# Kernel tuning notes

Hardware: AMD Instinct MI355X
Metric: run time of the kernel (lower is better)

The kernel has to match this reference:

```python
import jax, jax.numpy as jnp
import numpy as np

PC_RANGE = [-51.2, -51.2, -5.0, 51.2, 51.2, 3.0]
VOXEL = [0.1, 0.1, 0.2]
OSF = 8
NUM_PRIOR = 100
C = 256
BN_EPS = 1e-5
LN_EPS = 1e-5


def _conv(x, w, pad):
    # x: [B,C,H,W], w: [O,I,kh,kw]
    return jax.lax.conv_general_dilated(
        x, w, window_strides=(1, 1), padding=[(pad, pad), (pad, pad)],
        dimension_numbers=('NCHW', 'OIHW', 'NCHW'))


def _bn(x, g, b, m, v):
    scale = (g / jnp.sqrt(v + BN_EPS))[None, :, None, None]
    return (x - m[None, :, None, None]) * scale + b[None, :, None, None]


def setup_inputs() -> dict:
    key = jax.random.key(0)
    ks = jax.random.split(key, 24)
    s3 = 1.0 / np.sqrt(C * 9)
    s1 = 1.0 / np.sqrt(C)
    inp = {
        'bev_feat': jax.random.normal(ks[0], (4, C, 128, 128), jnp.float32),
        'template_anchor': jax.random.normal(ks[1], (4, 900, 11), jnp.float32),
        # shared_conv: 3x3 conv (no bias) + BN(eval) + ReLU
        'shared_w': jax.random.normal(ks[2], (C, C, 3, 3), jnp.float32) * s3,
        'bn1_g': jax.random.normal(ks[3], (C,), jnp.float32) * 0.1 + 1.0,
        'bn1_b': jax.random.normal(ks[4], (C,), jnp.float32) * 0.1,
        'bn1_m': jax.random.normal(ks[5], (C,), jnp.float32) * 0.1,
        'bn1_v': jax.random.uniform(ks[6], (C,), jnp.float32) + 0.5,
        # objectness: 3x3 conv (no bias) + BN + ReLU + 1x1 conv (bias=-2)
        'obj_w1': jax.random.normal(ks[7], (C, C, 3, 3), jnp.float32) * s3,
        'bn2_g': jax.random.normal(ks[8], (C,), jnp.float32) * 0.1 + 1.0,
        'bn2_b': jax.random.normal(ks[9], (C,), jnp.float32) * 0.1,
        'bn2_m': jax.random.normal(ks[10], (C,), jnp.float32) * 0.1,
        'bn2_v': jax.random.uniform(ks[11], (C,), jnp.float32) + 0.5,
        'obj_w2': jax.random.normal(ks[12], (1, C, 1, 1), jnp.float32) * s1,
        'obj_b2': jnp.full((1,), -2.0, jnp.float32),
        # feat_proj: Linear + LN + ReLU + Linear
        'fp_w1': jax.random.normal(ks[13], (C, C), jnp.float32) * s1,
        'fp_b1': jax.random.normal(ks[14], (C,), jnp.float32) * 0.01,
        'ln_g': jnp.ones((C,), jnp.float32),
        'ln_b': jnp.zeros((C,), jnp.float32),
        'fp_w2': jax.random.normal(ks[15], (C, C), jnp.float32) * s1,
        'fp_b2': jax.random.normal(ks[16], (C,), jnp.float32) * 0.01,
        # geometry heads (1x1 convs, bias init 0)
        'z_w': jax.random.normal(ks[17], (1, C, 1, 1), jnp.float32) * s1,
        'z_b': jnp.zeros((1,), jnp.float32),
        'dim_w': jax.random.normal(ks[18], (3, C, 1, 1), jnp.float32) * s1,
        'dim_b': jnp.zeros((3,), jnp.float32),
        'yaw_w': jax.random.normal(ks[19], (2, C, 1, 1), jnp.float32) * s1,
        'yaw_b': jnp.zeros((2,), jnp.float32),
        'vel_w': jax.random.normal(ks[20], (2, C, 1, 1), jnp.float32) * s1,
        'vel_b': jnp.zeros((2,), jnp.float32),
    }
    return inp


def _forward(bev_feat, template_anchor, shared_w, bn1_g, bn1_b, bn1_m, bn1_v,
             obj_w1, bn2_g, bn2_b, bn2_m, bn2_v, obj_w2, obj_b2,
             fp_w1, fp_b1, ln_g, ln_b, fp_w2, fp_b2,
             z_w, z_b, dim_w, dim_b, yaw_w, yaw_b, vel_w, vel_b):
    B, Cc, H, W = bev_feat.shape
    # shared_conv
    feat = jax.nn.relu(_bn(_conv(bev_feat, shared_w, 1), bn1_g, bn1_b, bn1_m, bn1_v))
    # objectness heatmap
    h = jax.nn.relu(_bn(_conv(feat, obj_w1, 1), bn2_g, bn2_b, bn2_m, bn2_v))
    heatmap = jax.nn.sigmoid(_conv(h, obj_w2, 0) + obj_b2[None, :, None, None])
    score = heatmap.reshape(B, H * W)
    K = min(NUM_PRIOR, H * W, template_anchor.shape[1])
    topk_score, topk_inds = jax.lax.top_k(score, K)  # [B,K]
    ys = topk_inds // W
    xs = topk_inds % W
    # gather BEV features at topk locations: [B,K,C]
    feat_flat = feat.reshape(B, Cc, H * W).transpose(0, 2, 1)
    gathered = jnp.take_along_axis(feat_flat, topk_inds[:, :, None], axis=1)
    # feat_proj: Linear + LN + ReLU + Linear
    x = gathered @ fp_w1.T + fp_b1
    mu = jnp.mean(x, axis=-1, keepdims=True)
    var = jnp.mean((x - mu) ** 2, axis=-1, keepdims=True)
    x = (x - mu) / jnp.sqrt(var + LN_EPS) * ln_g + ln_b
    x = jax.nn.relu(x)
    prior_feature = x @ fp_w2.T + fp_b2
    prior_feature = prior_feature * (1.0 + topk_score[:, :, None])
    # geometry heads (1x1 convs == linear on gathered features)
    z_pred = gathered @ z_w[:, :, 0, 0].T + z_b      # [B,K,1]
    dim_pred = gathered @ dim_w[:, :, 0, 0].T + dim_b  # [B,K,3]
    yaw_pred = gathered @ yaw_w[:, :, 0, 0].T + yaw_b  # [B,K,2]
    vel_pred = gathered @ vel_w[:, :, 0, 0].T + vel_b  # [B,K,2]
    # anchor update
    pa = template_anchor[:, :K, :]
    x_metric = (xs.astype(pa.dtype) + 0.5) * (VOXEL[0] * OSF) + PC_RANGE[0]
    y_metric = (ys.astype(pa.dtype) + 0.5) * (VOXEL[1] * OSF) + PC_RANGE[1]
    z_new = pa[..., 2] + 0.5 * z_pred[..., 0]
    dims_new = pa[..., 3:6] + 0.2 * jnp.clip(dim_pred, -1.0, 1.0)
    yaw = jnp.tanh(yaw_pred)
    nrm = jnp.maximum(jnp.sqrt(jnp.sum(yaw * yaw, axis=-1, keepdims=True)), 1e-6)
    yaw_new = 0.7 * pa[..., 6:8] + 0.3 * (yaw / nrm)
    vel_new = pa[..., 8:10] + 0.2 * jnp.clip(vel_pred, -2.0, 2.0)
    prior_anchor = jnp.concatenate([
        x_metric[..., None], y_metric[..., None], z_new[..., None],
        dims_new, yaw_new, vel_new, pa[..., 10:]], axis=-1)
    return prior_feature, prior_anchor, topk_score


def reference(bev_feat, template_anchor, shared_w, bn1_g, bn1_b, bn1_m, bn1_v,
              obj_w1, bn2_g, bn2_b, bn2_m, bn2_v, obj_w2, obj_b2,
              fp_w1, fp_b1, ln_g, ln_b, fp_w2, fp_b2,
              z_w, z_b, dim_w, dim_b, yaw_w, yaw_b, vel_w, vel_b):
    return _forward(bev_feat, template_anchor, shared_w, bn1_g, bn1_b, bn1_m, bn1_v,
                    obj_w1, bn2_g, bn2_b, bn2_m, bn2_v, obj_w2, obj_b2,
                    fp_w1, fp_b1, ln_g, ln_b, fp_w2, fp_b2,
                    z_w, z_b, dim_w, dim_b, yaw_w, yaw_b, vel_w, vel_b)
```

## Files before the change

### kernel.cpp

```cpp
#include <hip/hip_runtime.h>
#include <math.h>


typedef __attribute__((ext_vector_type(8))) short bf16x8;
typedef __attribute__((ext_vector_type(4))) float f32x4;

#define HW 16384
#define WPITCH 130
#define CCAP 192
#define PSTR 28
#define WSO_XN    0ULL
#define WSO_FEATB 34078720ULL
#define WSO_WP1   68157440ULL
#define WSO_WP2   69337088ULL
#define WSO_BNP   70516736ULL
#define WSO_LOG   70521856ULL
#define WSO_CAND  70784000ULL
#define WSO_CNT   70787072ULL
#define WSO_EXL   70787136ULL
#define WSO_TIDX  70790208ULL
#define WSO_TLOG  70791808ULL
#define WSO_W1N   70793408ULL
#define WSO_W2N   73152704ULL
#define WSO_A1P   WSO_XN
#define WSO_ACC2  28311552ULL

__device__ __forceinline__ float bf2f(short s) {
  return __uint_as_float(((unsigned)(unsigned short)s) << 16);
}
__device__ __forceinline__ short f2bf(float f) {
  unsigned u = __float_as_uint(f);
  u += 0x7fffu + ((u >> 16) & 1u);
  return (short)(u >> 16);
}
__device__ __forceinline__ void gll16(const void* g, void* l) {
  __builtin_amdgcn_global_load_lds(
      (const __attribute__((address_space(1))) void*)g,
      (__attribute__((address_space(3))) void*)l, 16, 0, 0);
}

__global__ void wprep2(const float* __restrict__ s1, const float* __restrict__ s2,
                       short* __restrict__ wp1, short* __restrict__ wp2,
                       float* __restrict__ wn1, float* __restrict__ wn2) {
  int bx = blockIdx.x;
  const float* src;
  short* wp;
  float* wn;
  if (bx >= 2304) {
    src = s2; wp = wp2; wn = wn2; bx -= 2304;
  } else {
    src = s1; wp = wp1; wn = wn1;
  }
  int i = bx * 256 + threadIdx.x;
  float v = src[i];
  int k = i % 9;
  int r = i / 9;
  int ci = r & 255;
  int co = r >> 8;
  wp[(k * 256 + co) * 256 + ci] = f2bf(v);
  wn[(ci * 9 + k) * 256 + co] = v;
}

__global__ void smallprep(const float* g1, const float* b1, const float* m1,
                          const float* v1, const float* g2, const float* b2,
                          const float* m2, const float* v2, const float* w2,
                          const float* ob2, float* __restrict__ bnp,
                          short* __restrict__ xn, short* __restrict__ featb,
                          float* __restrict__ logits) {
  const int blk = blockIdx.x, t = threadIdx.x;
  if (blk < 1024) {
    int i = blk * 256 + t;
    int c = i & 255;
    int r = i >> 8;
    int nh = r >> 1;
    int side = r & 1;
    size_t off = ((size_t)nh * WPITCH + (side ? 129 : 0)) * 256 + c;
    xn[off] = 0;
    featb[off] = 0;
  } else if (blk < 1280) {
    logits[(blk - 1024) * 256 + t] = ob2[0];
  } else {
    float s1 = g1[t] / sqrtf(v1[t] + 1e-5f);
    bnp[t] = s1;
    bnp[256 + t] = b1[t] - m1[t] * s1;
    float s2 = g2[t] / sqrtf(v2[t] + 1e-5f);
    bnp[512 + t] = s2;
    bnp[768 + t] = b2[t] - m2[t] * s2;
    bnp[1024 + t] = w2[t];
  }
}

__global__ __launch_bounds__(256) void nchw2nhwc(const float* __restrict__ in,
                                                 short* __restrict__ out) {
  __shared__ short tl[64 * 66];
  int n = blockIdx.z, c0 = blockIdx.y * 64, s0 = blockIdx.x * 64;
  int sl = threadIdx.x & 63, cl = threadIdx.x >> 6;
  for (int p = 0; p < 16; ++p) {
    int c = cl + p * 4;
    tl[c * 66 + sl] = f2bf(in[(((size_t)(n * 256 + c0 + c)) << 14) + s0 + sl]);
  }
  __syncthreads();
  int co = threadIdx.x & 63, so = threadIdx.x >> 6;
  for (int p = 0; p < 16; ++p) {
    int S = s0 + so + p * 4;
    int h = S >> 7, w = S & 127;
    out[(((size_t)(n * 128 + h)) * WPITCH + w + 1) * 256 + c0 + co] =
        tl[co * 66 + (so + p * 4)];
  }
}

template <int OUT_LOGITS>
__global__ __launch_bounds__(256) void conv3x3(const short* __restrict__ inp,
                                               const short* __restrict__ wp,
                                               const float* __restrict__ scale,
                                               const float* __restrict__ shift,
                                               const float* __restrict__ w2f,
                                               short* __restrict__ outb,
                                               float* __restrict__ logits) {
  __shared__ short a_sm[132 * 32];
  __shared__ short b_sm[3][128 * 32];
  const int t = threadIdx.x;
  const int wv = t >> 6, lane = t & 63;
  const int l15 = lane & 15, quad = lane >> 4;
  const int tile = blockIdx.x;
  const int img = tile >> 7;
  const int h = tile & 127;
  const int nblk = blockIdx.y;
  const int m0 = (wv & 1) << 6;
  const int n0 = (wv >> 1) << 6;

  f32x4 acc[4][4];
#pragma unroll
  for (int i = 0; i < 4; ++i)
#pragma unroll
    for (int j = 0; j < 4; ++j) {
      acc[i][j][0] = 0.f; acc[i][j][1] = 0.f;
      acc[i][j][2] = 0.f; acc[i][j][3] = 0.f;
    }

  for (int dhi = 0; dhi < 3; ++dhi) {
    const int hy = h + dhi - 1;
    if (hy < 0 || hy > 127) continue;
    const size_t arow = ((size_t)(img * 128 + hy)) * WPITCH;
    const short* wbase = wp + ((size_t)(dhi * 3 * 256 + nblk * 128)) * 256;

    for (int c0 = 0; c0 < 256; c0 += 32) {
      __syncthreads();
#pragma unroll
      for (int j = 0; j < 2; ++j) {
        const int seg = (j << 6) + (t >> 2);
        const int cc = t & 3;
        gll16(inp + (arow + seg) * 256 + c0 + cc * 8,
              a_sm + ((size_t)((j << 8) + t)) * 8);
      }
      if (t < 32) {
        const int r = t >> 4, dw = t & 15;
        const int* gsrc = (const int*)(inp + (arow + 128 + r) * 256 + c0) + dw;
        ((int*)a_sm)[(128 + r) * 16 + dw] = *gsrc;
      }
#pragma unroll
      for (int dwi = 0; dwi < 3; ++dwi) {
        const short* wtap = wbase + (size_t)dwi * 65536;
#pragma unroll
        for (int j = 0; j < 2; ++j) {
          const int nrow = (j << 6) + (t >> 2);
          const int cc = t & 3;
          gll16(wtap + (size_t)nrow * 256 + c0 + cc * 8,
                b_sm[dwi] + ((size_t)((j << 8) + t)) * 8);
        }
      }
      __syncthreads();

#pragma unroll
      for (int dwi = 0; dwi < 3; ++dwi) {
        bf16x8 af[4], bfr[4];
#pragma unroll
        for (int i = 0; i < 4; ++i)
          af[i] = *(const bf16x8*)(a_sm + (dwi + m0 + i * 16 + l15) * 32 + quad * 8);
#pragma unroll
        for (int i = 0; i < 4; ++i)
          bfr[i] = *(const bf16x8*)(b_sm[dwi] + (n0 + i * 16 + l15) * 32 + quad * 8);
#pragma unroll
        for (int i = 0; i < 4; ++i)
#pragma unroll
          for (int j = 0; j < 4; ++j)
            acc[i][j] = __builtin_amdgcn_mfma_f32_16x16x32_bf16(af[i], bfr[j],
                                                                acc[i][j], 0, 0, 0);
      }
    }
  }

  float sc[4], sh[4], wf[4];
#pragma unroll
  for (int j = 0; j < 4; ++j) {
    const int co = nblk * 128 + n0 + j * 16 + l15;
    sc[j] = scale[co];
    sh[j] = shift[co];
    if (OUT_LOGITS) wf[j] = w2f[co];
  }
  if (OUT_LOGITS) {
    float* lrow = logits + ((size_t)img << 14) + (h << 7);
#pragma unroll
    for (int i = 0; i < 4; ++i) {
#pragma unroll
      for (int r = 0; r < 4; ++r) {
        float part = 0.f;
#pragma unroll
        for (int j = 0; j < 4; ++j) {
          float v = fmaxf(acc[i][j][r] * sc[j] + sh[j], 0.f);
          part += v * wf[j];
        }
        part += __shfl_xor(part, 1);
        part += __shfl_xor(part, 2);
        part += __shfl_xor(part, 4);
        part += __shfl_xor(part, 8);
        if (l15 == 0)
          atomicAdd(&lrow[m0 + i * 16 + quad * 4 + r], part);
      }
    }
  } else {
    const size_t obase = ((size_t)(img * 128 + h)) * WPITCH + 1;
#pragma unroll
    for (int i = 0; i < 4; ++i) {
#pragma unroll
      for (int j = 0; j < 4; ++j) {
        const int co = nblk * 128 + n0 + j * 16 + l15;
#pragma unroll
        for (int r = 0; r < 4; ++r) {
          const int m = m0 + i * 16 + quad * 4 + r;
          float v = fmaxf(acc[i][j][r] * sc[j] + sh[j], 0.f);
          outb[(obase + m) * 256 + co] = f2bf(v);
        }
      }
    }
  }
}

__global__ __launch_bounds__(1024) void topk_radix(const float* __restrict__ logits,
                                                   int* __restrict__ cand,
                                                   int* __restrict__ cnt_out) {
  __shared__ int hist[2048];
  __shared__ int wsum[16];
  __shared__ unsigned sel_bin;
  __shared__ int sel_above;
  __shared__ int cntr;
  const int b = blockIdx.x, t = threadIdx.x;
  const int lane = t & 63, wid = t >> 6;
  const float* L = logits + (size_t)b * HW;
  const int base = t * 16;
  unsigned kv[16];
#pragma unroll
  for (int i = 0; i < 4; ++i) {
    float4 v = *(const float4*)(L + base + i * 4);
    float f4[4] = {v.x, v.y, v.z, v.w};
#pragma unroll
    for (int j = 0; j < 4; ++j) {
      unsigned u = __float_as_uint(f4[j]);
      kv[i * 4 + j] = u ^ (((unsigned)((int)u >> 31)) | 0x80000000u);
    }
  }
  unsigned prefix = 0, pmask = 0;
  int need = 128;
  const int shifts[3] = {21, 10, 0};
  const int nbs[3] = {2048, 2048, 1024};

  for (int lev = 0; lev < 3; ++lev) {
    const int shift = shifts[lev];
    const int nb = nbs[lev];
    hist[t] = 0;
    hist[t + 1024] = 0;
    __syncthreads();
#pragma unroll
    for (int i = 0; i < 16; ++i)
      if ((kv[i] & pmask) == prefix)
        atomicAdd(&hist[(kv[i] >> shift) & (nb - 1)], 1);
    __syncthreads();
    const int cs = nb >> 10;
    const int bin_hi = nb - 1 - t * cs;
    const int c_hi = hist[bin_hi];
    const int c_lo = (cs == 2) ? hist[bin_hi - 1] : 0;
    const int s = c_hi + c_lo;
    int inc = s;
    for (int off = 1; off < 64; off <<= 1) {
      int nbr = __shfl_up(inc, off);
      if (lane >= off) inc += nbr;
    }
    if (lane == 63) wsum[wid] = inc;
    __syncthreads();
    if (wid == 0) {
      int wv = (lane < 16) ? wsum[lane] : 0;
      for (int off = 1; off < 16; off <<= 1) {
        int nbr = __shfl_up(wv, off);
        if (lane >= off) wv += nbr;
      }
      if (lane < 16) wsum[lane] = wv;
    }
    __syncthreads();
    const int excl = inc - s + (wid ? wsum[wid - 1] : 0);
    if (excl < need && need <= excl + s) {
      if (need <= excl + c_hi) {
        sel_bin = (unsigned)bin_hi;
        sel_above = excl;
      } else {
        sel_bin = (unsigned)(bin_hi - 1);
        sel_above = excl + c_hi;
      }
    }
    __syncthreads();
    prefix |= sel_bin << shift;
    pmask |= ((unsigned)(nb - 1)) << shift;
    need -= sel_above;
    __syncthreads();
  }
  if (t == 0) cntr = 0;
  __syncthreads();
#pragma unroll
  for (int i = 0; i < 16; ++i) {
    if (kv[i] >= prefix) {
      int p = atomicAdd(&cntr, 1);
      if (p < CCAP) cand[b * CCAP + p] = base + i;
    }
  }
  __syncthreads();
  if (t == 0) cnt_out[b] = (cntr < CCAP) ? cntr : CCAP;
}

__global__ __launch_bounds__(256) void rescore_a(const float* __restrict__ bev,
                                                 const float* __restrict__ w1n,
                                                 const int* __restrict__ cand,
                                                 const int* __restrict__ cnt,
                                                 float* __restrict__ a1part) {
  const int bx = blockIdx.x, b = blockIdx.y, z = blockIdx.z;
  const int t = threadIdx.x;
  const int n = cnt[b];
  const int c0 = bx * 4;
  if (c0 >= n) return;
  const int nc = (n - c0 < 4) ? (n - c0) : 4;
  const int ci0 = z << 6;
  __shared__ float patch[4 * 64 * PSTR];

  {
    const int TE = nc * 1600;
    int sg[4];
#pragma unroll
    for (int g = 0; g < 4; ++g) {
      int cc = c0 + g;
      sg[g] = cand[b * CCAP + ((cc < n) ? cc : (n - 1))];
    }
#pragma unroll
    for (int k = 0; k < 25; ++k) {
      int e = t + (k << 8);
      if (e < TE) {
        int g = (e >= 3200) ? ((e >= 4800) ? 3 : 2) : ((e >= 1600) ? 1 : 0);
        int rem = e - g * 1600;
        int ci = rem / 25;
        int rj = rem - ci * 25;
        int r = rj / 5;
        int j = rj - r * 5;
        int s = sg[g];
        int hy = (s >> 7) - 2 + r, wx = (s & 127) - 2 + j;
        float v = 0.f;
        if (hy >= 0 && hy < 128 && wx >= 0 && wx < 128)
          v = bev[(((size_t)(b * 256 + ci0 + ci)) << 14) + (hy << 7) + wx];
        patch[(g * 64 + ci) * PSTR + rj] = v;
      } else {
        int g2 = (e >= 3200) ? ((e >= 4800) ? 3 : 2) : 1;
        int rem = e - g2 * 1600;
        int ci = rem / 25;
        int rj = rem - ci * 25;
        patch[(g2 * 64 + ci) * PSTR + rj] = 0.f;
      }
    }
  }
  __syncthreads();

  const int co = t;
  float a[4][9];
#pragma unroll
  for (int g = 0; g < 4; ++g)
#pragma unroll
    for (int p = 0; p < 9; ++p) a[g][p] = 0.f;

  for (int ci = 0; ci < 64; ++ci) {
    const float* wr = w1n + (size_t)(ci0 + ci) * 2304 + co;
    float w9[9];
#pragma unroll
    for (int k = 0; k < 9; ++k) w9[k] = wr[k * 256];
#pragma unroll
    for (int g = 0; g < 4; ++g) {
      const float4* pr = (const float4*)(patch + (g * 64 + ci) * PSTR);
      float xp[28];
#pragma unroll
      for (int q = 0; q < 7; ++q) {
        float4 v = pr[q];
        xp[q * 4 + 0] = v.x; xp[q * 4 + 1] = v.y;
        xp[q * 4 + 2] = v.z; xp[q * 4 + 3] = v.w;
      }
#pragma unroll
      for (int py = 0; py < 3; ++py)
#pragma unroll
        for (int px = 0; px < 3; ++px)
#pragma unroll
          for (int ky = 0; ky < 3; ++ky)
#pragma unroll
            for (int kx = 0; kx < 3; ++kx)
              a[g][py * 3 + px] += w9[ky * 3 + kx] * xp[(py + ky) * 5 + px + kx];
    }
  }

#pragma unroll
  for (int g = 0; g < 4; ++g) {
    if (g < nc) {
      float* dst =
          a1part + ((((size_t)(b * CCAP + c0 + g) * 4 + z) * 9) << 8) + co;
#pragma unroll
      for (int p = 0; p < 9; ++p) dst[p << 8] = a[g][p];
    }
  }
}

__global__ __launch_bounds__(256) void rescore_b(const float* __restrict__ a1part,
                                                 const float* __restrict__ w2n,
                                                 const float* __restrict__ bnp,
                                                 const int* __restrict__ cnt,
                                                 float* __restrict__ acc2) {
  const int bx = blockIdx.x, b = blockIdx.y, z = blockIdx.z;
  const int t = threadIdx.x;
  const int n = cnt[b];
  const int cbase = bx * 8;
  if (cbase >= n) return;
  const int zb = z << 6;
  __shared__ float f9[8 * 64 * 12];

  const int cf = t & 63;
  const int pg = t >> 6;
  const int cfg = zb + cf;
  const float sc1 = bnp[cfg], sh1 = bnp[256 + cfg];
#pragma unroll
  for (int g = 0; g < 8; ++g) {
    const int c = cbase + g;
    if (c < n) {
      const float* src =
          a1part + ((((size_t)(b * CCAP + c)) * 36) << 8) + cfg;
      for (int p = pg; p < 9; p += 4) {
        float v = src[(size_t)(0 * 9 + p) << 8] + src[(size_t)(1 * 9 + p) << 8] +
                  src[(size_t)(2 * 9 + p) << 8] + src[(size_t)(3 * 9 + p) << 8];
        f9[(g * 64 + cf) * 12 + p] = fmaxf(v * sc1 + sh1, 0.f);
      }
    } else {
      for (int p = pg; p < 9; p += 4) f9[(g * 64 + cf) * 12 + p] = 0.f;
    }
  }
  __syncthreads();

  float acc[8];
#pragma unroll
  for (int g = 0; g < 8; ++g) acc[g] = 0.f;
  for (int ci = 0; ci < 64; ++ci) {
    const float* wr = w2n + (size_t)(zb + ci) * 2304 + t;
    float w9[9];
#pragma unroll
    for (int k = 0; k < 9; ++k) w9[k] = wr[k * 256];
#pragma unroll
    for (int g = 0; g < 8; ++g) {
      const float4* fp = (const float4*)(f9 + (g * 64 + ci) * 12);
      float4 f0 = fp[0], f1 = fp[1], f2 = fp[2];
      acc[g] += w9[0] * f0.x;
      acc[g] += w9[1] * f0.y;
      acc[g] += w9[2] * f0.z;
      acc[g] += w9[3] * f0.w;
      acc[g] += w9[4] * f1.x;
      acc[g] += w9[5] * f1.y;
      acc[g] += w9[6] * f1.z;
      acc[g] += w9[7] * f1.w;
      acc[g] += w9[8] * f2.x;
    }
  }
#pragma unroll
  for (int g = 0; g < 8; ++g) {
    const int c = cbase + g;
    if (c < n)
      acc2[((((size_t)(b * CCAP + c)) * 4 + z) << 8) + t] = acc[g];
  }
}

__global__ __launch_bounds__(256) void rescore_c(const float* __restrict__ acc2,
                                                 const float* __restrict__ bnp,
                                                 const float* __restrict__ b2,
                                                 const int* __restrict__ cnt,
                                                 float* __restrict__ exlog) {
  const int bx = blockIdx.x, b = blockIdx.y, t = threadIdx.x;
  const int lane = t & 63, wid = t >> 6;
  const int n = cnt[b];
  const int c = bx * 4 + wid;
  if (c >= n) return;
  const float* src = acc2 + (((size_t)(b * CCAP + c)) << 10);
  float p = 0.f;
#pragma unroll
  for (int j = 0; j < 4; ++j) {
    const int co = lane + j * 64;
    float v = ((src[co] + src[256 + co]) + src[512 + co]) + src[768 + co];
    p += fmaxf(v * bnp[512 + co] + bnp[768 + co], 0.f) * bnp[1024 + co];
  }
  for (int off = 32; off; off >>= 1) p += __shfl_xor(p, off);
  if (lane == 0) exlog[b * CCAP + c] = p + b2[0];
}

__global__ __launch_bounds__(CCAP) void final_topk(const float* __restrict__ exlog,
                                                   const int* __restrict__ cand,
                                                   const int* __restrict__ cnt,
                                                   int* __restrict__ tidx,
                                                   float* __restrict__ tlog) {
  const int b = blockIdx.x, t = threadIdx.x;
  __shared__ float v[CCAP];
  __shared__ int si[CCAP];
  const int n = cnt[b];
  float mv = (t < n) ? exlog[b * CCAP + t] : -3.0e38f;
  int s = (t < n) ? cand[b * CCAP + t] : 0x7FFFFFFF;
  v[t] = mv;
  si[t] = s;
  __syncthreads();
  int rank = 0;
  for (int j = 0; j < CCAP; ++j) {
    float vj = v[j];
    int sj = si[j];
    if (vj > mv || (vj == mv && sj < s)) ++rank;
  }
  if (t < n && rank < 100) {
    tidx[b * 100 + rank] = s;
    tlog[b * 100 + rank] = mv;
  }
}

__global__ __launch_bounds__(256) void head_kern(
    const short* __restrict__ featb, const int* __restrict__ tidx,
    const float* __restrict__ tlog, const float* __restrict__ tmpl,
    const float* __restrict__ w1, const float* __restrict__ b1,
    const float* __restrict__ lng, const float* __restrict__ lnb,
    const float* __restrict__ w2, const float* __restrict__ b2,
    const float* __restrict__ zw, const float* __restrict__ zb,
    const float* __restrict__ dmw, const float* __restrict__ dmb,
    const float* __restrict__ yw, const float* __restrict__ yb,
    const float* __restrict__ vw, const float* __restrict__ vb,
    float* __restrict__ out) {
  const int blk = blockIdx.x;
  const int b = blk / 100, q = blk % 100;
  const int t = threadIdx.x;
  const int lane = t & 63, wid = t >> 6;
  __shared__ float g[256];
  __shared__ float sx[256];
  __shared__ float red[4];
  __shared__ float heads[8];

  const int s = tidx[b * 100 + q];
  const float score = 1.f / (1.f + expf(-tlog[b * 100 + q]));
  const int ys = s >> 7, xs = s & 127;

  g[t] = bf2f(featb[(((size_t)(b * 128 + ys)) * WPITCH + xs + 1) * 256 + t]);
  __syncthreads();

  float x = b1[t];
  {
    const float* wr = w1 + (size_t)t * 256;
    for (int i = 0; i < 256; i += 4) {
      float4 wv = *(const float4*)(wr + i);
      x += g[i] * wv.x + g[i + 1] * wv.y + g[i + 2] * wv.z + g[i + 3] * wv.w;
    }
  }
  float sum = x;
  for (int off = 32; off; off >>= 1) sum += __shfl_xor(sum, off);
  if (lane == 0) red[wid] = sum;
  __syncthreads();
  float mu = (red[0] + red[1] + red[2] + red[3]) * (1.f / 256.f);
  __syncthreads();
  float d = x - mu;
  float q2 = d * d;
  for (int off = 32; off; off >>= 1) q2 += __shfl_xor(q2, off);
  if (lane == 0) red[wid] = q2;
  __syncthreads();
  float var = (red[0] + red[1] + red[2] + red[3]) * (1.f / 256.f);
  float xn = d * (1.f / sqrtf(var + 1e-5f)) * lng[t] + lnb[t];
  xn = fmaxf(xn, 0.f);
  sx[t] = xn;
  __syncthreads();
  float pf = b2[t];
  {
    const float* wr = w2 + (size_t)t * 256;
    for (int i = 0; i < 256; i += 4) {
      float4 wv = *(const float4*)(wr + i);
      pf += sx[i] * wv.x + sx[i + 1] * wv.y + sx[i + 2] * wv.z + sx[i + 3] * wv.w;
    }
  }
  pf *= (1.f + score);
  out[(size_t)(b * 100 + q) * 256 + t] = pf;

  const int k = t >> 5, l = t & 31;
  const float* hw;
  float hb;
  if (k == 0)      { hw = zw;                 hb = zb[0]; }
  else if (k < 4)  { hw = dmw + (k - 1) * 256; hb = dmb[k - 1]; }
  else if (k < 6)  { hw = yw + (k - 4) * 256;  hb = yb[k - 4]; }
  else             { hw = vw + (k - 6) * 256;  hb = vb[k - 6]; }
  float hp = 0.f;
#pragma unroll
  for (int r = 0; r < 8; ++r) {
    int i = l + r * 32;
    hp += g[i] * hw[i];
  }
  for (int off = 16; off; off >>= 1) hp += __shfl_xor(hp, off);
  if (l == 0) heads[k] = hp + hb;
  __syncthreads();

  if (t == 0) {
    const float* pa = tmpl + ((size_t)b * 900 + q) * 11;
    float p[11];
#pragma unroll
    for (int i = 0; i < 11; ++i) p[i] = pa[i];
    float a[11];
    a[0] = ((float)xs + 0.5f) * 0.8f - 51.2f;
    a[1] = ((float)ys + 0.5f) * 0.8f - 51.2f;
    a[2] = p[2] + 0.5f * heads[0];
#pragma unroll
    for (int i = 0; i < 3; ++i)
      a[3 + i] = p[3 + i] + 0.2f * fminf(fmaxf(heads[1 + i], -1.f), 1.f);
    float t0 = tanhf(heads[4]), t1 = tanhf(heads[5]);
    float nrm = fmaxf(sqrtf(t0 * t0 + t1 * t1), 1e-6f);
    a[6] = 0.7f * p[6] + 0.3f * t0 / nrm;
    a[7] = 0.7f * p[7] + 0.3f * t1 / nrm;
    a[8] = p[8] + 0.2f * fminf(fmaxf(heads[6], -2.f), 2.f);
    a[9] = p[9] + 0.2f * fminf(fmaxf(heads[7], -2.f), 2.f);
    a[10] = p[10];
    float* oa = out + 102400 + (size_t)(b * 100 + q) * 11;
#pragma unroll
    for (int i = 0; i < 11; ++i) oa[i] = a[i];
    out[106800 + b * 100 + q] = score;
  }
}

extern "C" void kernel_launch(void* const* d_in, const int* in_sizes, int n_in,
                              void* d_out, int out_size, void* d_ws, size_t ws_size,
                              hipStream_t stream) {
  (void)in_sizes; (void)n_in; (void)out_size; (void)ws_size;
  char* ws = (char*)d_ws;
  short* xn     = (short*)(ws + WSO_XN);
  short* featb  = (short*)(ws + WSO_FEATB);
  short* wp1    = (short*)(ws + WSO_WP1);
  short* wp2    = (short*)(ws + WSO_WP2);
  float* bnp    = (float*)(ws + WSO_BNP);
  float* logits = (float*)(ws + WSO_LOG);
  int*   cand   = (int*)(ws + WSO_CAND);
  int*   cnt    = (int*)(ws + WSO_CNT);
  float* exl    = (float*)(ws + WSO_EXL);
  int*   tidx   = (int*)(ws + WSO_TIDX);
  float* tlog   = (float*)(ws + WSO_TLOG);
  float* w1n    = (float*)(ws + WSO_W1N);
  float* w2n    = (float*)(ws + WSO_W2N);
  float* a1p    = (float*)(ws + WSO_A1P);
  float* acc2   = (float*)(ws + WSO_ACC2);

  const float* bev = (const float*)d_in[0];

  wprep2<<<4608, 256, 0, stream>>>((const float*)d_in[2], (const float*)d_in[7],
                                   wp1, wp2, w1n, w2n);
  smallprep<<<1281, 256, 0, stream>>>(
      (const float*)d_in[3], (const float*)d_in[4], (const float*)d_in[5],
      (const float*)d_in[6], (const float*)d_in[8], (const float*)d_in[9],
      (const float*)d_in[10], (const float*)d_in[11], (const float*)d_in[12],
      (const float*)d_in[13], bnp, xn, featb, logits);
  nchw2nhwc<<<dim3(256, 4, 4), 256, 0, stream>>>(bev, xn);
  conv3x3<0><<<dim3(512, 2), 256, 0, stream>>>(xn, wp1, bnp, bnp + 256,
                                               nullptr, featb, nullptr);
  conv3x3<1><<<dim3(512, 2), 256, 0, stream>>>(featb, wp2, bnp + 512, bnp + 768,
                                               bnp + 1024, nullptr, logits);
  topk_radix<<<4, 1024, 0, stream>>>(logits, cand, cnt);
  rescore_a<<<dim3(CCAP / 4, 4, 4), 256, 0, stream>>>(bev, w1n, cand, cnt, a1p);
  rescore_b<<<dim3(CCAP / 8, 4, 4), 256, 0, stream>>>(a1p, w2n, bnp, cnt, acc2);
  rescore_c<<<dim3(CCAP / 4, 4), 256, 0, stream>>>(acc2, bnp,
                                                   (const float*)d_in[13], cnt,
                                                   exl);
  final_topk<<<4, CCAP, 0, stream>>>(exl, cand, cnt, tidx, tlog);
  head_kern<<<400, 256, 0, stream>>>(
      featb, tidx, tlog, (const float*)d_in[1],
      (const float*)d_in[14], (const float*)d_in[15], (const float*)d_in[16],
      (const float*)d_in[17], (const float*)d_in[18], (const float*)d_in[19],
      (const float*)d_in[20], (const float*)d_in[21], (const float*)d_in[22],
      (const float*)d_in[23], (const float*)d_in[24], (const float*)d_in[25],
      (const float*)d_in[26], (const float*)d_in[27], (float*)d_out);
}
```

Measured before the change: 564.9 us.

## Remap rescore_a threads to candidate×channel-quad with double-buffered weight loads

rescore_a now gives each wavefront a single candidate. Each thread accumulates four output channels spaced 64 apart, instead of one channel across four candidates. Patch values in LDS are now shared among four output channels per thread, and weight loads are software-pipelined across consecutive input channels with two register buffers. This reduces how often the same patch data is re-read from LDS. It also raises register pressure, so launch_bounds(256,2) is added. Wavefronts belonging to absent candidates (g >= nc) still compute, and their results are discarded.

Result: faster. 540.3 us (-4.4%).

```diff
diff --git a/kernel.cpp b/kernel.cpp
--- a/kernel.cpp
+++ b/kernel.cpp
@@ -325,11 +325,46 @@
   if (t == 0) cnt_out[b] = (cntr < CCAP) ? cntr : CCAP;
 }
 
-__global__ __launch_bounds__(256) void rescore_a(const float* __restrict__ bev,
-                                                 const float* __restrict__ w1n,
-                                                 const int* __restrict__ cand,
-                                                 const int* __restrict__ cnt,
-                                                 float* __restrict__ a1part) {
+__device__ __forceinline__ void wload4(const float* __restrict__ wr,
+                                       float w[4][9]) {
+#pragma unroll
+  for (int k = 0; k < 9; ++k)
+#pragma unroll
+    for (int h = 0; h < 4; ++h)
+      w[h][k] = wr[k * 256 + (h << 6)];
+}
+
+__device__ __forceinline__ void conv_step(const float* __restrict__ pc,
+                                          const float w[4][9], float a[4][9]) {
+  float xp[28];
+  const float4* pr = (const float4*)pc;
+#pragma unroll
+  for (int q = 0; q < 7; ++q) {
+    float4 v = pr[q];
+    xp[q * 4 + 0] = v.x; xp[q * 4 + 1] = v.y;
+    xp[q * 4 + 2] = v.z; xp[q * 4 + 3] = v.w;
+  }
+#pragma unroll
+  for (int py = 0; py < 3; ++py)
+#pragma unroll
+    for (int px = 0; px < 3; ++px)
+#pragma unroll
+      for (int ky = 0; ky < 3; ++ky)
+#pragma unroll
+        for (int kx = 0; kx < 3; ++kx) {
+          const float xv = xp[(py + ky) * 5 + px + kx];
+          const int pp = py * 3 + px, kk = ky * 3 + kx;
+          a[0][pp] += w[0][kk] * xv;
+          a[1][pp] += w[1][kk] * xv;
+          a[2][pp] += w[2][kk] * xv;
+          a[3][pp] += w[3][kk] * xv;
+        }
+}
+
+__global__ __launch_bounds__(256, 2) void rescore_a(
+    const float* __restrict__ bev, const float* __restrict__ w1n,
+    const int* __restrict__ cand, const int* __restrict__ cnt,
+    float* __restrict__ a1part) {
   const int bx = blockIdx.x, b = blockIdx.y, z = blockIdx.z;
   const int t = threadIdx.x;
   const int n = cnt[b];
@@ -364,58 +399,46 @@
           v = bev[(((size_t)(b * 256 + ci0 + ci)) << 14) + (hy << 7) + wx];
         patch[(g * 64 + ci) * PSTR + rj] = v;
       } else {
-        int g2 = (e >= 3200) ? ((e >= 4800) ? 3 : 2) : 1;
-        int rem = e - g2 * 1600;
+        int g2z = (e >= 3200) ? ((e >= 4800) ? 3 : 2) : 1;
+        int rem = e - g2z * 1600;
         int ci = rem / 25;
         int rj = rem - ci * 25;
-        patch[(g2 * 64 + ci) * PSTR + rj] = 0.f;
-      }
-    }
-  }
-  __syncthreads();
-
-  const int co = t;
+        patch[(g2z * 64 + ci) * PSTR + rj] = 0.f;
+      }
+    }
+  }
+  __syncthreads();
+
+  const int col = t & 63;
+  const int g = t >> 6;
   float a[4][9];
 #pragma unroll
-  for (int g = 0; g < 4; ++g)
-#pragma unroll
-    for (int p = 0; p < 9; ++p) a[g][p] = 0.f;
-
-  for (int ci = 0; ci < 64; ++ci) {
-    const float* wr = w1n + (size_t)(ci0 + ci) * 2304 + co;
-    float w9[9];
-#pragma unroll
-    for (int k = 0; k < 9; ++k) w9[k] = wr[k * 256];
-#pragma unroll
-    for (int g = 0; g < 4; ++g) {
-      const float4* pr = (const float4*)(patch + (g * 64 + ci) * PSTR);
-      float xp[28];
-#pragma unroll
-      for (int q = 0; q < 7; ++q) {
-        float4 v = pr[q];
-        xp[q * 4 + 0] = v.x; xp[q * 4 + 1] = v.y;
-        xp[q * 4 + 2] = v.z; xp[q * 4 + 3] = v.w;
-      }
-#pragma unroll
-      for (int py = 0; py < 3; ++py)
-#pragma unroll
-        for (int px = 0; px < 3; ++px)
-#pragma unroll
-          for (int ky = 0; ky < 3; ++ky)
-#pragma unroll
-            for (int kx = 0; kx < 3; ++kx)
-              a[g][py * 3 + px] += w9[ky * 3 + kx] * xp[(py + ky) * 5 + px + kx];
-    }
-  }
-
-#pragma unroll
-  for (int g = 0; g < 4; ++g) {
-    if (g < nc) {
-      float* dst =
-          a1part + ((((size_t)(b * CCAP + c0 + g) * 4 + z) * 9) << 8) + co;
-#pragma unroll
-      for (int p = 0; p < 9; ++p) dst[p << 8] = a[g][p];
-    }
+  for (int h = 0; h < 4; ++h)
+#pragma unroll
+    for (int p = 0; p < 9; ++p) a[h][p] = 0.f;
+
+  const float* pbase = patch + (g << 6) * PSTR;
+  const float* wbase = w1n + (size_t)ci0 * 2304 + col;
+
+  float wA[4][9], wB[4][9];
+  wload4(wbase, wA);
+  for (int ci = 0; ci < 64; ci += 2) {
+    wload4(wbase + (size_t)(ci + 1) * 2304, wB);
+    conv_step(pbase + ci * PSTR, wA, a);
+    if (ci + 2 < 64)
+      wload4(wbase + (size_t)(ci + 2) * 2304, wA);
+    conv_step(pbase + (ci + 1) * PSTR, wB, a);
+  }
+
+  if (g < nc) {
+    const int c = c0 + g;
+    float* dst =
+        a1part + ((((size_t)(b * CCAP + c) * 4 + z) * 9) << 8) + col;
+#pragma unroll
+    for (int p = 0; p < 9; ++p)
+#pragma unroll
+      for (int h = 0; h < 4; ++h)
+        dst[(p << 8) + (h << 6)] = a[h][p];
   }
 }
 
```
